# Kernel optimization log

Measured on AMD Instinct MI355X. Metric: run time of the kernel, lower is better.

Reference implementation:

```python
import jax, jax.numpy as jnp
import numpy as np

N_NODES = 50000
N_EDGES = 800000
N_GRAPHS = 256


def setup_inputs() -> dict:
    key = jax.random.key(0)
    ks = jax.random.split(key, 16)

    def w(k, shape):
        fan_in = shape[0]
        return (jax.random.normal(k, shape, jnp.float32) / np.sqrt(fan_in)).astype(jnp.float32)

    x = jax.random.normal(ks[0], (N_NODES, 19), jnp.float32)
    edge_index = jax.random.randint(ks[1], (2, N_EDGES), 0, N_NODES, dtype=jnp.int64)
    batch = jnp.sort(jax.random.randint(ks[2], (N_NODES,), 0, N_GRAPHS, dtype=jnp.int64))

    return {
        "x": x,
        "edge_index": edge_index,
        "batch": batch,
        "W1": w(ks[3], (19, 500)),  "b1": 0.01 * jax.random.normal(ks[4], (500,), jnp.float32),
        "W2": w(ks[5], (500, 400)), "b2": 0.01 * jax.random.normal(ks[6], (400,), jnp.float32),
        "W3": w(ks[7], (400, 300)), "b3": 0.01 * jax.random.normal(ks[8], (300,), jnp.float32),
        "Wl1": w(ks[9], (300, 200)),  "bl1": 0.01 * jax.random.normal(ks[10], (200,), jnp.float32),
        "Wl2": w(ks[11], (200, 100)), "bl2": 0.01 * jax.random.normal(ks[12], (100,), jnp.float32),
        "Wl3": w(ks[13], (100, 6)),   "bl3": 0.01 * jax.random.normal(ks[14], (6,), jnp.float32),
    }


def _gcn_conv(h, src, dst, W, b, n_nodes):
    # PyG GCNConv: linear transform, then sym-normalized aggregation with self-loops.
    h = h @ W                                   # [N, out]
    deg = jnp.zeros((n_nodes,), h.dtype).at[dst].add(1.0) + 1.0  # +1 self-loop
    dinv = jax.lax.rsqrt(deg)
    coef = dinv[src] * dinv[dst]                # [E]
    agg = jax.ops.segment_sum(h[src] * coef[:, None], dst, num_segments=n_nodes)
    agg = agg + h * (dinv * dinv)[:, None]      # self-loop contribution
    return agg + b


def reference(x, edge_index, batch, W1, b1, W2, b2, W3, b3,
              Wl1, bl1, Wl2, bl2, Wl3, bl3):
    src, dst = edge_index[0], edge_index[1]
    n = x.shape[0]
    h = jax.nn.relu(_gcn_conv(x, src, dst, W1, b1, n))
    h = jax.nn.relu(_gcn_conv(h, src, dst, W2, b2, n))
    # dropout p=0.3 is identity in eval mode
    h = jax.nn.relu(_gcn_conv(h, src, dst, W3, b3, n))
    # MaxAggregation by graph id
    g = jax.ops.segment_max(h, batch, num_segments=N_GRAPHS)  # [G, 300]
    g = jax.nn.relu(g @ Wl1 + bl1)
    g = jax.nn.relu(g @ Wl2 + bl2)
    logits = g @ Wl3 + bl3                       # [G, 6]
    # faithful to source: softmax over dim=0 (graph axis)
    return jax.nn.softmax(logits, axis=0)
```

## Files before the change

kernel.cpp:

```cpp
#include <hip/hip_runtime.h>
#include <hip/hip_bf16.h>

#define NN 50000
#define NNP 50016
#define NE 800000
#define NG 256
#define NB_SCAN 196

typedef __attribute__((ext_vector_type(8))) short short8;
typedef __attribute__((ext_vector_type(8))) unsigned short ushort8;
typedef __attribute__((ext_vector_type(4))) float f32x4;

struct __align__(8) Edge { int s; float c; };

__device__ __forceinline__ float u2f(unsigned short u) {
  unsigned int t = ((unsigned int)u) << 16;
  return __builtin_bit_cast(float, t);
}
__device__ __forceinline__ unsigned short f2b(float f) {
  __hip_bfloat16 b = __float2bfloat16(f);
  return __builtin_bit_cast(unsigned short, b);
}
__device__ __forceinline__ f32x4 mfma_bf16(short8 a, short8 b, f32x4 c) {
  return __builtin_amdgcn_mfma_f32_16x16x32_bf16(a, b, c, 0, 0, 0);
}
__device__ __forceinline__ void fma8(float* acc, float c, const ushort8& v) {
  #pragma unroll
  for (int j = 0; j < 8; j++) acc[j] += c * u2f(v[j]);
}

#define GRAMP(vv, cc, S, E0, CNT, BASE, STRIDE)                         \
  if ((S) < (CNT)) { Edge ed = ecs[(E0) + (S)]; cc = ed.c;              \
    vv = *(const ushort8*)((BASE) + (size_t)ed.s * (STRIDE) + cb); }    \
  else { cc = 0.f; vv = (ushort8)0; }

#define GSTEP(vv, cc, acc, EOFF, E0, E1, CNT, BASE, STRIDE)             \
  { ushort8 tv = vv; float tc = cc; int en = (E0) + (EOFF) + 4;         \
    if (en < (E1)) { Edge ed = ecs[en]; cc = ed.c;                      \
      vv = *(const ushort8*)((BASE) + (size_t)ed.s * (STRIDE) + cb); }  \
    if ((EOFF) < (CNT)) fma8(acc, tc, tv); }

__global__ void k_zero_i32(int* __restrict__ p, int n) {
  int i = blockIdx.x * blockDim.x + threadIdx.x;
  if (i < n) p[i] = 0;
}
__global__ void k_count(const int* __restrict__ dst, int* __restrict__ counts, int E) {
  int e = blockIdx.x * blockDim.x + threadIdx.x;
  if (e < E) atomicAdd(&counts[dst[e]], 1);
}
__global__ void k_dinv(const int* __restrict__ counts, float* __restrict__ dinv,
                       float* __restrict__ selfc, int n) {
  int i = blockIdx.x * blockDim.x + threadIdx.x;
  if (i < n) {
    float d = (float)counts[i] + 1.0f;
    dinv[i]  = rsqrtf(d);
    selfc[i] = 1.0f / d;
  }
}

__global__ void k_scan1(const int* __restrict__ counts, int* __restrict__ row_ptr,
                        int* __restrict__ bsum) {
  __shared__ int ws[4];
  int tid = threadIdx.x;
  int i = blockIdx.x * 256 + tid;
  int v = (i < NN) ? counts[i] : 0;
  int incl = v;
  #pragma unroll
  for (int off = 1; off < 64; off <<= 1) {
    int t = __shfl_up(incl, off, 64);
    if ((tid & 63) >= off) incl += t;
  }
  int wv = tid >> 6;
  if ((tid & 63) == 63) ws[wv] = incl;
  __syncthreads();
  if (tid == 0) {
    int s0 = ws[0], s1 = ws[1], s2 = ws[2], s3 = ws[3];
    ws[0] = 0; ws[1] = s0; ws[2] = s0 + s1; ws[3] = s0 + s1 + s2;
    bsum[blockIdx.x] = s0 + s1 + s2 + s3;
  }
  __syncthreads();
  if (i < NN) row_ptr[i] = ws[wv] + incl - v;
}
__global__ void k_scan2(int* __restrict__ bsum, int* __restrict__ row_ptr) {
  __shared__ int ws[4];
  int tid = threadIdx.x;
  int v = (tid < NB_SCAN) ? bsum[tid] : 0;
  int incl = v;
  #pragma unroll
  for (int off = 1; off < 64; off <<= 1) {
    int t = __shfl_up(incl, off, 64);
    if ((tid & 63) >= off) incl += t;
  }
  int wv = tid >> 6;
  if ((tid & 63) == 63) ws[wv] = incl;
  __syncthreads();
  if (tid == 0) {
    int s0 = ws[0], s1 = ws[1], s2 = ws[2], s3 = ws[3];
    ws[0] = 0; ws[1] = s0; ws[2] = s0 + s1; ws[3] = s0 + s1 + s2;
    row_ptr[NN] = s0 + s1 + s2 + s3;
  }
  __syncthreads();
  if (tid < NB_SCAN) bsum[tid] = ws[wv] + incl - v;
}
__global__ void k_scan3(const int* __restrict__ bsum, int* __restrict__ row_ptr,
                        int* __restrict__ fill) {
  int i = blockIdx.x * 256 + threadIdx.x;
  if (i < NN) {
    row_ptr[i] += bsum[blockIdx.x];
    fill[i] = 0;
  }
}

__global__ void k_fill(const int* __restrict__ src, const int* __restrict__ dst,
                       const int* __restrict__ row_ptr, int* __restrict__ fill,
                       const float* __restrict__ dinv, Edge* __restrict__ ecs, int E) {
  int e = blockIdx.x * blockDim.x + threadIdx.x;
  if (e < E) {
    int s = src[e], d = dst[e];
    int pos = row_ptr[d] + atomicAdd(&fill[d], 1);
    Edge ed; ed.s = s; ed.c = dinv[s] * dinv[d];
    ecs[pos] = ed;
  }
}

#define PR_W1 16384
#define PR_W2 212992
#define PR_W3 133120
#define PR_B1 512
#define PR_GB 76800
__global__ void k_prep_all(const float* __restrict__ W1, const float* __restrict__ W2,
                           const float* __restrict__ W3, const float* __restrict__ b1,
                           unsigned short* __restrict__ W1t, unsigned short* __restrict__ W2t,
                           unsigned short* __restrict__ W3t, float* __restrict__ b1p,
                           float* __restrict__ gbuf) {
  int idx = blockIdx.x * blockDim.x + threadIdx.x;
  if (idx < PR_W1) {
    int n = idx >> 5, k = idx & 31;
    W1t[idx] = f2b((n < 500 && k < 19) ? W1[k * 500 + n] : 0.f);
    return;
  }
  idx -= PR_W1;
  if (idx < PR_W2) {
    int n = idx >> 9, k = idx & 511;
    W2t[idx] = f2b((n < 400 && k < 500) ? W2[k * 400 + n] : 0.f);
    return;
  }
  idx -= PR_W2;
  if (idx < PR_W3) {
    int n = idx / 416, k = idx - n * 416;
    W3t[idx] = f2b((n < 300 && k < 400) ? W3[k * 300 + n] : 0.f);
    return;
  }
  idx -= PR_W3;
  if (idx < PR_B1) { b1p[idx] = (idx < 500) ? b1[idx] : 0.f; return; }
  idx -= PR_B1;
  if (idx < PR_GB) gbuf[idx] = 0.f;
}

__global__ __launch_bounds__(256, 4) void k_agg_x(
    const float* __restrict__ x, const int* __restrict__ row_ptr,
    const Edge* __restrict__ ecs, const float* __restrict__ selfc,
    unsigned short* __restrict__ aggxb, int n) {
  int tid  = threadIdx.x;
  int node = blockIdx.x * 8 + (tid >> 5);
  int lane = tid & 31;
  if (node >= NNP) return;
  float acc = 0.f;
  if (node < n && lane < 19) {
    int e0 = row_ptr[node], e1 = row_ptr[node + 1];
    int cnt = e1 - e0;
    float v0 = 0.f, v1 = 0.f, v2 = 0.f, v3 = 0.f;
    float c0 = 0.f, c1 = 0.f, c2 = 0.f, c3 = 0.f;
    if (cnt > 0) { Edge ed = ecs[e0];     c0 = ed.c; v0 = x[(size_t)ed.s * 19 + lane]; }
    if (cnt > 1) { Edge ed = ecs[e0 + 1]; c1 = ed.c; v1 = x[(size_t)ed.s * 19 + lane]; }
    if (cnt > 2) { Edge ed = ecs[e0 + 2]; c2 = ed.c; v2 = x[(size_t)ed.s * 19 + lane]; }
    if (cnt > 3) { Edge ed = ecs[e0 + 3]; c3 = ed.c; v3 = x[(size_t)ed.s * 19 + lane]; }
    for (int e = 0; e < cnt; e += 4) {
      float tv, tc; int en;
      tv = v0; tc = c0; en = e0 + e + 4;
      if (en < e1) { Edge ed = ecs[en]; c0 = ed.c; v0 = x[(size_t)ed.s * 19 + lane]; }
      if (e < cnt) acc += tc * tv;
      tv = v1; tc = c1; en = e0 + e + 5;
      if (en < e1) { Edge ed = ecs[en]; c1 = ed.c; v1 = x[(size_t)ed.s * 19 + lane]; }
      if (e + 1 < cnt) acc += tc * tv;
      tv = v2; tc = c2; en = e0 + e + 6;
      if (en < e1) { Edge ed = ecs[en]; c2 = ed.c; v2 = x[(size_t)ed.s * 19 + lane]; }
      if (e + 2 < cnt) acc += tc * tv;
      tv = v3; tc = c3; en = e0 + e + 7;
      if (en < e1) { Edge ed = ecs[en]; c3 = ed.c; v3 = x[(size_t)ed.s * 19 + lane]; }
      if (e + 3 < cnt) acc += tc * tv;
    }
    acc += selfc[node] * x[(size_t)node * 19 + lane];
  }
  aggxb[(size_t)node * 32 + lane] = (node < n && lane < 19) ? f2b(acc) : (unsigned short)0;
}

__global__ __launch_bounds__(256) void k_fused12(
    const unsigned short* __restrict__ aggxb, const unsigned short* __restrict__ W1t,
    const float* __restrict__ b1p, const unsigned short* __restrict__ W2t,
    unsigned short* __restrict__ T2) {
  __shared__ unsigned short Hs[32][520];
  int tid = threadIdx.x;
  int lane = tid & 63, wv = tid >> 6;
  int l15 = lane & 15, quad = lane >> 4;
  int r0 = blockIdx.x * 32;
  for (int t = wv; t < 64; t += 4) {
    int rt = t & 1, ct = t >> 1;
    short8 a = *(const short8*)(aggxb + (size_t)(r0 + rt * 16 + l15) * 32 + quad * 8);
    short8 b = *(const short8*)(W1t + (size_t)(ct * 16 + l15) * 32 + quad * 8);
    f32x4 c = {0.f, 0.f, 0.f, 0.f};
    c = mfma_bf16(a, b, c);
    int col = ct * 16 + l15;
    float bias = b1p[col];
    int rbase = rt * 16 + quad * 4;
    #pragma unroll
    for (int r = 0; r < 4; r++)
      Hs[rbase + r][col] = f2b(fmaxf(c[r] + bias, 0.f));
  }
  __syncthreads();
  int rt = wv >> 1, p = wv & 1;
  f32x4 acc[13];
  #pragma unroll
  for (int j = 0; j < 13; j++) acc[j] = (f32x4){0.f, 0.f, 0.f, 0.f};
  for (int k0 = 0; k0 < 512; k0 += 32) {
    short8 a = *(const short8*)&Hs[rt * 16 + l15][k0 + quad * 8];
    #pragma unroll
    for (int j = 0; j < 13; j++) {
      int n = (p + 2 * j) * 16 + l15;
      short8 b = *(const short8*)(W2t + (size_t)n * 512 + k0 + quad * 8);
      acc[j] = mfma_bf16(a, b, acc[j]);
    }
  }
  int rr = r0 + rt * 16 + quad * 4;
  #pragma unroll
  for (int j = 0; j < 13; j++) {
    int n = (p + 2 * j) * 16 + l15;
    if (n < 400) {
      #pragma unroll
      for (int r = 0; r < 4; r++) {
        int row = rr + r;
        if (row < NN) T2[(size_t)row * 400 + n] = f2b(acc[j][r]);
      }
    }
  }
}

__global__ __launch_bounds__(256, 4) void k_fused23(
    const unsigned short* __restrict__ T2, const int* __restrict__ row_ptr,
    const Edge* __restrict__ ecs, const float* __restrict__ selfc,
    const float* __restrict__ b2, const unsigned short* __restrict__ W3t,
    unsigned short* __restrict__ T3) {
  __shared__ unsigned short Hs[32][424];
  int tid = threadIdx.x;
  int lane = tid & 63, wv = tid >> 6;
  int l15 = lane & 15, quad = lane >> 4;
  int r0 = blockIdx.x * 32;
  bool act = lane < 50;
  int cb = lane * 8;
  for (int i = 0; i < 8; i++) {
    int nl = wv + 4 * i;
    int node = r0 + nl;
    ushort8 out = (ushort8)0;
    if (node < NN && act) {
      float acc[8];
      #pragma unroll
      for (int j = 0; j < 8; j++) acc[j] = 0.f;
      int e0 = row_ptr[node], e1 = row_ptr[node + 1];
      int cnt = e1 - e0;
      ushort8 v0, v1, v2, v3;
      float c0, c1, c2, c3;
      GRAMP(v0, c0, 0, e0, cnt, T2, 400)
      GRAMP(v1, c1, 1, e0, cnt, T2, 400)
      GRAMP(v2, c2, 2, e0, cnt, T2, 400)
      GRAMP(v3, c3, 3, e0, cnt, T2, 400)
      for (int e = 0; e < cnt; e += 4) {
        GSTEP(v0, c0, acc, e + 0, e0, e1, cnt, T2, 400)
        GSTEP(v1, c1, acc, e + 1, e0, e1, cnt, T2, 400)
        GSTEP(v2, c2, acc, e + 2, e0, e1, cnt, T2, 400)
        GSTEP(v3, c3, acc, e + 3, e0, e1, cnt, T2, 400)
      }
      ushort8 sv = *(const ushort8*)(T2 + (size_t)node * 400 + cb);
      float sc = selfc[node];
      #pragma unroll
      for (int j = 0; j < 8; j++)
        out[j] = f2b(fmaxf(acc[j] + sc * u2f(sv[j]) + b2[cb + j], 0.f));
    }
    if (lane < 52) *(ushort8*)&Hs[nl][cb] = out;
  }
  __syncthreads();
  int rt = wv >> 1, p = wv & 1;
  f32x4 acc[10];
  #pragma unroll
  for (int j = 0; j < 10; j++) acc[j] = (f32x4){0.f, 0.f, 0.f, 0.f};
  for (int k0 = 0; k0 < 416; k0 += 32) {
    short8 a = *(const short8*)&Hs[rt * 16 + l15][k0 + quad * 8];
    #pragma unroll
    for (int j = 0; j < 10; j++) {
      int n = (p + 2 * j) * 16 + l15;
      short8 b = *(const short8*)(W3t + (size_t)n * 416 + k0 + quad * 8);
      acc[j] = mfma_bf16(a, b, acc[j]);
    }
  }
  int rr = r0 + rt * 16 + quad * 4;
  #pragma unroll
  for (int j = 0; j < 10; j++) {
    int n = (p + 2 * j) * 16 + l15;
    if (n < 300) {
      #pragma unroll
      for (int r = 0; r < 4; r++) {
        int row = rr + r;
        if (row < NN) T3[(size_t)row * 304 + n] = f2b(acc[j][r]);
      }
    }
  }
}

__global__ __launch_bounds__(256, 4) void k_fused3m(
    const unsigned short* __restrict__ T3, const int* __restrict__ row_ptr,
    const Edge* __restrict__ ecs, const float* __restrict__ selfc,
    const float* __restrict__ b3, const int* __restrict__ batch,
    float* __restrict__ gbuf) {
  __shared__ unsigned int lmax[4][304];
  int tid = threadIdx.x;
  int lane = tid & 63, wv = tid >> 6;
  int r0 = blockIdx.x * 32;
  int g0 = batch[r0];
  for (int i = tid; i < 4 * 304; i += 256) ((unsigned int*)lmax)[i] = 0u;
  __syncthreads();
  bool act = lane < 38;
  int cb = lane * 8;
  for (int i = 0; i < 8; i++) {
    int node = r0 + wv * 8 + i;
    if (node >= NN) break;
    if (act) {
      float acc[8];
      #pragma unroll
      for (int j = 0; j < 8; j++) acc[j] = 0.f;
      int e0 = row_ptr[node], e1 = row_ptr[node + 1];
      int cnt = e1 - e0;
      ushort8 v0, v1, v2, v3;
      float c0, c1, c2, c3;
      GRAMP(v0, c0, 0, e0, cnt, T3, 304)
      GRAMP(v1, c1, 1, e0, cnt, T3, 304)
      GRAMP(v2, c2, 2, e0, cnt, T3, 304)
      GRAMP(v3, c3, 3, e0, cnt, T3, 304)
      for (int e = 0; e < cnt; e += 4) {
        GSTEP(v0, c0, acc, e + 0, e0, e1, cnt, T3, 304)
        GSTEP(v1, c1, acc, e + 1, e0, e1, cnt, T3, 304)
        GSTEP(v2, c2, acc, e + 2, e0, e1, cnt, T3, 304)
        GSTEP(v3, c3, acc, e + 3, e0, e1, cnt, T3, 304)
      }
      ushort8 sv = *(const ushort8*)(T3 + (size_t)node * 304 + cb);
      float sc = selfc[node];
      int slot = batch[node] - g0;
      #pragma unroll
      for (int j = 0; j < 8; j++) {
        int c = cb + j;
        if (c < 300) {
          float v = fmaxf(acc[j] + sc * u2f(sv[j]) + b3[c], 0.f);
          unsigned int uv = __float_as_uint(v);
          if (slot < 4) atomicMax(&lmax[slot][c], uv);
          else atomicMax((unsigned int*)&gbuf[(size_t)(g0 + slot) * 300 + c], uv);
        }
      }
    }
  }
  __syncthreads();
  for (int i = tid; i < 4 * 304; i += 256) {
    int s = i / 304, c = i - s * 304;
    unsigned int uv = lmax[s][c];
    int g = g0 + s;
    if (c < 300 && uv != 0u && g < NG)
      atomicMax((unsigned int*)&gbuf[(size_t)g * 300 + c], uv);
  }
}

__global__ __launch_bounds__(256) void k_head(
    const float* __restrict__ gbuf, const float* __restrict__ Wl1,
    const float* __restrict__ bl1, const float* __restrict__ Wl2,
    const float* __restrict__ bl2, const float* __restrict__ Wl3,
    const float* __restrict__ bl3, float* __restrict__ logits) {
  __shared__ float g[304], a1[200], a2[112];
  int gid = blockIdx.x, tid = threadIdx.x;
  for (int i = tid; i < 300; i += 256) g[i] = gbuf[(size_t)gid * 300 + i];
  __syncthreads();
  if (tid < 200) {
    float acc = bl1[tid];
    for (int k = 0; k < 300; k++) acc += g[k] * Wl1[k * 200 + tid];
    a1[tid] = fmaxf(acc, 0.f);
  }
  __syncthreads();
  if (tid < 100) {
    float acc = bl2[tid];
    for (int k = 0; k < 200; k++) acc += a1[k] * Wl2[k * 100 + tid];
    a2[tid] = fmaxf(acc, 0.f);
  }
  __syncthreads();
  if (tid < 6) {
    float acc = bl3[tid];
    for (int k = 0; k < 100; k++) acc += a2[k] * Wl3[k * 6 + tid];
    logits[gid * 6 + tid] = acc;
  }
}

__global__ void k_softmax0(const float* __restrict__ logits, float* __restrict__ out) {
  __shared__ float cmax[6], csum[6];
  int g = threadIdx.x;
  if (g < 6) {
    float m = -1e30f;
    for (int i = 0; i < NG; i++) m = fmaxf(m, logits[i * 6 + g]);
    float s = 0.f;
    for (int i = 0; i < NG; i++) s += expf(logits[i * 6 + g] - m);
    cmax[g] = m; csum[g] = s;
  }
  __syncthreads();
  for (int c = 0; c < 6; c++)
    out[g * 6 + c] = expf(logits[g * 6 + c] - cmax[c]) / csum[c];
}

extern "C" void kernel_launch(void* const* d_in, const int* in_sizes, int n_in,
                              void* d_out, int out_size, void* d_ws, size_t ws_size,
                              hipStream_t stream) {
  const float* x    = (const float*)d_in[0];
  const int*   eidx = (const int*)d_in[1];
  const int*   batch= (const int*)d_in[2];
  const float* W1 = (const float*)d_in[3];  const float* b1 = (const float*)d_in[4];
  const float* W2 = (const float*)d_in[5];  const float* b2 = (const float*)d_in[6];
  const float* W3 = (const float*)d_in[7];  const float* b3 = (const float*)d_in[8];
  const float* Wl1= (const float*)d_in[9];  const float* bl1= (const float*)d_in[10];
  const float* Wl2= (const float*)d_in[11]; const float* bl2= (const float*)d_in[12];
  const float* Wl3= (const float*)d_in[13]; const float* bl3= (const float*)d_in[14];
  const int* srcA = eidx;
  const int* dstA = eidx + NE;

  char* ws = (char*)d_ws;
  size_t off = 0;
  auto alloc = [&](size_t bytes) -> char* {
    char* p = ws + off;
    off = (off + bytes + 255) & ~(size_t)255;
    return p;
  };
  int*   counts  = (int*)  alloc((size_t)NN * 4);
  int*   row_ptr = (int*)  alloc((size_t)(NN + 1) * 4);
  int*   fill    = (int*)  alloc((size_t)NN * 4);
  int*   bsum    = (int*)  alloc(256 * 4);
  float* dinv    = (float*)alloc((size_t)NN * 4);
  float* selfc   = (float*)alloc((size_t)NN * 4);
  Edge*  ecs     = (Edge*) alloc((size_t)NE * 8);
  unsigned short* aggxb = (unsigned short*)alloc((size_t)NNP * 32 * 2);
  unsigned short* W1t   = (unsigned short*)alloc((size_t)512 * 32 * 2);
  unsigned short* W2t   = (unsigned short*)alloc((size_t)416 * 512 * 2);
  unsigned short* W3t   = (unsigned short*)alloc((size_t)320 * 416 * 2);
  float* b1p     = (float*)alloc(512 * 4);
  unsigned short* T2 = (unsigned short*)alloc((size_t)NNP * 400 * 2);
  unsigned short* T3 = (unsigned short*)alloc((size_t)NNP * 304 * 2);
  float* gbuf    = (float*)alloc((size_t)NG * 300 * 4);
  float* logits  = (float*)alloc((size_t)NG * 6 * 4);

  k_zero_i32<<<(NN + 255) / 256, 256, 0, stream>>>(counts, NN);
  k_count<<<(NE + 255) / 256, 256, 0, stream>>>(dstA, counts, NE);
  k_dinv<<<(NN + 255) / 256, 256, 0, stream>>>(counts, dinv, selfc, NN);
  k_scan1<<<NB_SCAN, 256, 0, stream>>>(counts, row_ptr, bsum);
  k_scan2<<<1, 256, 0, stream>>>(bsum, row_ptr);
  k_scan3<<<NB_SCAN, 256, 0, stream>>>(bsum, row_ptr, fill);
  k_fill<<<(NE + 255) / 256, 256, 0, stream>>>(srcA, dstA, row_ptr, fill, dinv, ecs, NE);
  k_prep_all<<<(PR_W1 + PR_W2 + PR_W3 + PR_B1 + PR_GB + 255) / 256, 256, 0, stream>>>(
      W1, W2, W3, b1, W1t, W2t, W3t, b1p, gbuf);
  k_agg_x<<<(NNP + 7) / 8, 256, 0, stream>>>(x, row_ptr, ecs, selfc, aggxb, NN);
  k_fused12<<<NNP / 32, 256, 0, stream>>>(aggxb, W1t, b1p, W2t, T2);
  k_fused23<<<NNP / 32, 256, 0, stream>>>(T2, row_ptr, ecs, selfc, b2, W3t, T3);
  k_fused3m<<<NNP / 32, 256, 0, stream>>>(T3, row_ptr, ecs, selfc, b3, batch, gbuf);
  k_head<<<NG, 256, 0, stream>>>(gbuf, Wl1, bl1, Wl2, bl2, Wl3, bl3, logits);
  k_softmax0<<<1, 256, 0, stream>>>(logits, (float*)d_out);
}
```

Baseline: 747.0 us.

## Stage K-chunked weight tiles in LDS for both fused GEMM kernels

The prep kernel now writes W2 and W3 in a K-chunked layout: 32-wide K slices, each holding contiguous rows for every output column. The fused12 and fused23 kernels load each chunk cooperatively into a padded shared-memory tile (row stride 34), and MFMA B operands are read from LDS instead of from global memory per wave. This aims to remove redundant global/L2 reads of weights by waves that share the same columns. In exchange it adds two block barriers per K-chunk with no double buffering, and raises LDS use, which may lower occupancy. The 68-byte row stride also means the 16-byte LDS accesses are not 16-byte aligned.

```diff
diff --git a/kernel.cpp b/kernel.cpp
--- a/kernel.cpp
+++ b/kernel.cpp
@@ -130,8 +130,8 @@
 #define PR_GB 76800
 __global__ void k_prep_all(const float* __restrict__ W1, const float* __restrict__ W2,
                            const float* __restrict__ W3, const float* __restrict__ b1,
-                           unsigned short* __restrict__ W1t, unsigned short* __restrict__ W2t,
-                           unsigned short* __restrict__ W3t, float* __restrict__ b1p,
+                           unsigned short* __restrict__ W1t, unsigned short* __restrict__ W2c,
+                           unsigned short* __restrict__ W3c, float* __restrict__ b1p,
                            float* __restrict__ gbuf) {
   int idx = blockIdx.x * blockDim.x + threadIdx.x;
   if (idx < PR_W1) {
@@ -142,13 +142,17 @@
   idx -= PR_W1;
   if (idx < PR_W2) {
     int n = idx >> 9, k = idx & 511;
-    W2t[idx] = f2b((n < 400 && k < 500) ? W2[k * 400 + n] : 0.f);
+    float v = (n < 400 && k < 500) ? W2[k * 400 + n] : 0.f;
+    int ch = k >> 5, kk = k & 31;
+    W2c[((size_t)ch * 416 + n) * 32 + kk] = f2b(v);
     return;
   }
   idx -= PR_W2;
   if (idx < PR_W3) {
     int n = idx / 416, k = idx - n * 416;
-    W3t[idx] = f2b((n < 300 && k < 400) ? W3[k * 300 + n] : 0.f);
+    float v = (n < 300 && k < 400) ? W3[k * 300 + n] : 0.f;
+    int ch = k >> 5, kk = k & 31;
+    W3c[((size_t)ch * 320 + n) * 32 + kk] = f2b(v);
     return;
   }
   idx -= PR_W3;
@@ -197,9 +201,10 @@
 
 __global__ __launch_bounds__(256) void k_fused12(
     const unsigned short* __restrict__ aggxb, const unsigned short* __restrict__ W1t,
-    const float* __restrict__ b1p, const unsigned short* __restrict__ W2t,
+    const float* __restrict__ b1p, const unsigned short* __restrict__ W2c,
     unsigned short* __restrict__ T2) {
   __shared__ unsigned short Hs[32][520];
+  __shared__ unsigned short Ws[416 * 34];
   int tid = threadIdx.x;
   int lane = tid & 63, wv = tid >> 6;
   int l15 = lane & 15, quad = lane >> 4;
@@ -217,17 +222,28 @@
     for (int r = 0; r < 4; r++)
       Hs[rbase + r][col] = f2b(fmaxf(c[r] + bias, 0.f));
   }
-  __syncthreads();
   int rt = wv >> 1, p = wv & 1;
   f32x4 acc[13];
   #pragma unroll
   for (int j = 0; j < 13; j++) acc[j] = (f32x4){0.f, 0.f, 0.f, 0.f};
-  for (int k0 = 0; k0 < 512; k0 += 32) {
-    short8 a = *(const short8*)&Hs[rt * 16 + l15][k0 + quad * 8];
+  for (int ch = 0; ch < 16; ch++) {
+    __syncthreads();
+    const unsigned short* src = W2c + (size_t)ch * (416 * 32);
+    #pragma unroll
+    for (int it = 0; it < 7; it++) {
+      int idx = it * 256 + tid;
+      if (idx < 1664) {
+        ushort8 v = *(const ushort8*)(src + idx * 8);
+        int n = idx >> 2, part = idx & 3;
+        *(ushort8*)&Ws[n * 34 + part * 8] = v;
+      }
+    }
+    __syncthreads();
+    short8 a = *(const short8*)&Hs[rt * 16 + l15][ch * 32 + quad * 8];
     #pragma unroll
     for (int j = 0; j < 13; j++) {
       int n = (p + 2 * j) * 16 + l15;
-      short8 b = *(const short8*)(W2t + (size_t)n * 512 + k0 + quad * 8);
+      short8 b = *(const short8*)&Ws[n * 34 + quad * 8];
       acc[j] = mfma_bf16(a, b, acc[j]);
     }
   }
@@ -248,9 +264,10 @@
 __global__ __launch_bounds__(256, 4) void k_fused23(
     const unsigned short* __restrict__ T2, const int* __restrict__ row_ptr,
     const Edge* __restrict__ ecs, const float* __restrict__ selfc,
-    const float* __restrict__ b2, const unsigned short* __restrict__ W3t,
+    const float* __restrict__ b2, const unsigned short* __restrict__ W3c,
     unsigned short* __restrict__ T3) {
   __shared__ unsigned short Hs[32][424];
+  __shared__ unsigned short Ws[320 * 34];
   int tid = threadIdx.x;
   int lane = tid & 63, wv = tid >> 6;
   int l15 = lane & 15, quad = lane >> 4;
@@ -287,17 +304,26 @@
     }
     if (lane < 52) *(ushort8*)&Hs[nl][cb] = out;
   }
-  __syncthreads();
   int rt = wv >> 1, p = wv & 1;
   f32x4 acc[10];
   #pragma unroll
   for (int j = 0; j < 10; j++) acc[j] = (f32x4){0.f, 0.f, 0.f, 0.f};
-  for (int k0 = 0; k0 < 416; k0 += 32) {
-    short8 a = *(const short8*)&Hs[rt * 16 + l15][k0 + quad * 8];
+  for (int ch = 0; ch < 13; ch++) {
+    __syncthreads();
+    const unsigned short* src = W3c + (size_t)ch * (320 * 32);
+    #pragma unroll
+    for (int it = 0; it < 5; it++) {
+      int idx = it * 256 + tid;
+      ushort8 v = *(const ushort8*)(src + idx * 8);
+      int n = idx >> 2, part = idx & 3;
+      *(ushort8*)&Ws[n * 34 + part * 8] = v;
+    }
+    __syncthreads();
+    short8 a = *(const short8*)&Hs[rt * 16 + l15][ch * 32 + quad * 8];
     #pragma unroll
     for (int j = 0; j < 10; j++) {
       int n = (p + 2 * j) * 16 + l15;
-      short8 b = *(const short8*)(W3t + (size_t)n * 416 + k0 + quad * 8);
+      short8 b = *(const short8*)&Ws[n * 34 + quad * 8];
       acc[j] = mfma_bf16(a, b, acc[j]);
     }
   }
@@ -449,8 +475,8 @@
   Edge*  ecs     = (Edge*) alloc((size_t)NE * 8);
   unsigned short* aggxb = (unsigned short*)alloc((size_t)NNP * 32 * 2);
   unsigned short* W1t   = (unsigned short*)alloc((size_t)512 * 32 * 2);
-  unsigned short* W2t   = (unsigned short*)alloc((size_t)416 * 512 * 2);
-  unsigned short* W3t   = (unsigned short*)alloc((size_t)320 * 416 * 2);
+  unsigned short* W2c   = (unsigned short*)alloc((size_t)416 * 512 * 2);
+  unsigned short* W3c   = (unsigned short*)alloc((size_t)320 * 416 * 2);
   float* b1p     = (float*)alloc(512 * 4);
   unsigned short* T2 = (unsigned short*)alloc((size_t)NNP * 400 * 2);
   unsigned short* T3 = (unsigned short*)alloc((size_t)NNP * 304 * 2);
@@ -465,10 +491,10 @@
   k_scan3<<<NB_SCAN, 256, 0, stream>>>(bsum, row_ptr, fill);
   k_fill<<<(NE + 255) / 256, 256, 0, stream>>>(srcA, dstA, row_ptr, fill, dinv, ecs, NE);
   k_prep_all<<<(PR_W1 + PR_W2 + PR_W3 + PR_B1 + PR_GB + 255) / 256, 256, 0, stream>>>(
-      W1, W2, W3, b1, W1t, W2t, W3t, b1p, gbuf);
+      W1, W2, W3, b1, W1t, W2c, W3c, b1p, gbuf);
   k_agg_x<<<(NNP + 7) / 8, 256, 0, stream>>>(x, row_ptr, ecs, selfc, aggxb, NN);
-  k_fused12<<<NNP / 32, 256, 0, stream>>>(aggxb, W1t, b1p, W2t, T2);
-  k_fused23<<<NNP / 32, 256, 0, stream>>>(T2, row_ptr, ecs, selfc, b2, W3t, T3);
+  k_fused12<<<NNP / 32, 256, 0, stream>>>(aggxb, W1t, b1p, W2c, T2);
+  k_fused23<<<NNP / 32, 256, 0, stream>>>(T2, row_ptr, ecs, selfc, b2, W3c, T3);
   k_fused3m<<<NNP / 32, 256, 0, stream>>>(T3, row_ptr, ecs, selfc, b3, batch, gbuf);
   k_head<<<NG, 256, 0, stream>>>(gbuf, Wl1, bl1, Wl2, bl2, Wl3, bl3, logits);
   k_softmax0<<<1, 256, 0, stream>>>(logits, (float*)d_out);
```

After: 718.5 us. 1.04x faster.
